# Optimization experiments

Hardware: AMD Instinct MI355X
Metric: run time of the kernel (lower is better)

The kernel has to match this reference:

```python
import jax, jax.numpy as jnp
import numpy as np

D_MODEL = 1024
N_HEADS = 16
HEAD_DIM = D_MODEL // N_HEADS


def setup_inputs() -> dict:
    key = jax.random.key(0)
    ks = jax.random.split(key, 6)
    B, S = 4, 2048
    query = jax.random.normal(ks[0], (B, S, D_MODEL), dtype=jnp.float32)
    key_value = jax.random.normal(ks[1], (B, S, D_MODEL), dtype=jnp.float32)
    scale = 1.0 / np.sqrt(D_MODEL)
    Wq = jax.random.normal(ks[2], (D_MODEL, D_MODEL), dtype=jnp.float32) * scale
    Wk = jax.random.normal(ks[3], (D_MODEL, D_MODEL), dtype=jnp.float32) * scale
    Wv = jax.random.normal(ks[4], (D_MODEL, D_MODEL), dtype=jnp.float32) * scale
    Wo = jax.random.normal(ks[5], (D_MODEL, D_MODEL), dtype=jnp.float32) * scale
    return {"query": query, "key_value": key_value, "Wq": Wq, "Wk": Wk, "Wv": Wv, "Wo": Wo}


def reference(query, key_value, Wq, Wk, Wv, Wo):
    B, S, _ = query.shape
    H, Dh = N_HEADS, HEAD_DIM
    # nn.Linear (no bias): y = x @ W.T ; then split heads -> [B, H, S, Dh]
    q = (query @ Wq.T).reshape(B, S, H, Dh).transpose(0, 2, 1, 3)
    k = (key_value @ Wk.T).reshape(B, S, H, Dh).transpose(0, 2, 1, 3)
    v = (key_value @ Wv.T).reshape(B, S, H, Dh).transpose(0, 2, 1, 3)
    scale = Dh ** -0.5
    scores = jnp.einsum("bhqd,bhkd->bhqk", q, k) * scale  # [B,H,S,S]
    causal = jnp.tril(jnp.ones((S, S), dtype=bool))  # True where allowed
    scores = jnp.where(causal, scores, -jnp.inf)
    attn = jax.nn.softmax(scores, axis=-1)
    out = jnp.einsum("bhqk,bhkd->bhqd", attn, v)  # [B,H,S,Dh]
    out = out.transpose(0, 2, 1, 3).reshape(B, S, H * Dh)
    return out @ Wo.T
```

## Files before the change

### kernel.cpp

```cpp
#include <hip/hip_runtime.h>
#include <stdint.h>

typedef unsigned short u16;
typedef __attribute__((ext_vector_type(4))) unsigned short u16x4;
typedef __attribute__((ext_vector_type(8))) unsigned short u16x8;
typedef __attribute__((ext_vector_type(8))) __bf16 bf16x8;
typedef __attribute__((ext_vector_type(2))) _Float16 half2;
typedef __attribute__((ext_vector_type(8))) _Float16 half8;
typedef __attribute__((ext_vector_type(4))) float f32x4;

#define SEQ 2048
#define DM 1024
#define NH 16
#define DH 64
#define BATCH 4
#define MROWS (BATCH * SEQ)
#define NKT 16

#define SC_LOG2E 0.18033688011112042f

__device__ __forceinline__ u16 f2bf(float f) {
    uint32_t u = __builtin_bit_cast(uint32_t, f);
    u += 0x7fffu + ((u >> 16) & 1u);
    return (u16)(u >> 16);
}
__device__ __forceinline__ u16 f2h(float f) {
    return __builtin_bit_cast(u16, (_Float16)f);
}
__device__ __forceinline__ half2 pkrtz(float a, float b) {
    return __builtin_bit_cast(half2, __builtin_amdgcn_cvt_pkrtz(a, b));
}

__device__ __forceinline__ void load16_lds(const void* g, void* l) {
    __builtin_amdgcn_global_load_lds(
        (const __attribute__((address_space(1))) uint32_t*)(uintptr_t)g,
        (__attribute__((address_space(3))) uint32_t*)(uintptr_t)l,
        16, 0, 0);
}

#define N4A (MROWS * DM / 4)
#define N4W (DM * DM / 4)

__device__ __forceinline__ void cvt_one(const float* src, u16* dst, int i) {
    float4 v = ((const float4*)src)[i];
    u16x4 o;
    o[0] = f2bf(v.x); o[1] = f2bf(v.y); o[2] = f2bf(v.z); o[3] = f2bf(v.w);
    *(u16x4*)(dst + (size_t)i * 4) = o;
}

__global__ void cvt_all(const float* __restrict__ q, const float* __restrict__ kv,
                        const float* __restrict__ w0, const float* __restrict__ w1,
                        const float* __restrict__ w2, const float* __restrict__ w3,
                        u16* __restrict__ dq, u16* __restrict__ dkv,
                        u16* __restrict__ dw0, u16* __restrict__ dw1,
                        u16* __restrict__ dw2, u16* __restrict__ dw3) {
    int i = blockIdx.x * 256 + threadIdx.x;
    if (i < N4A) { cvt_one(q, dq, i); return; }
    i -= N4A;
    if (i < N4A) { cvt_one(kv, dkv, i); return; }
    i -= N4A;
    int s = i >> 18;
    int l = i & (N4W - 1);
    const float* src = s == 0 ? w0 : s == 1 ? w1 : s == 2 ? w2 : w3;
    u16* dst = s == 0 ? dw0 : s == 1 ? dw1 : s == 2 ? dw2 : dw3;
    cvt_one(src, dst, l);
}

#define LDS_DB 24576
#define LDS_AH 8192
#define LDS_BH 4096

__device__ __forceinline__ void gemm_core(const u16* __restrict__ Ag,
                                          const u16* __restrict__ Bg,
                                          int m0, int n0, f32x4 (&acc)[4][4]) {
    __shared__ __align__(16) u16 lds[2 * LDS_DB];
    const int t = threadIdx.x;
    const int lane = t & 63;
    const int w = t >> 6;
    const int ln = lane & 15, quad = lane >> 4;
    const int wml = (w >> 1) * 64;
    const int wnl = (w & 1) * 64;
    const int rowT = t >> 2;
    const int cswz8 = (((t & 3) ^ ((t >> 3) & 3)) << 3);
    const int swz = ((quad ^ ((ln >> 1) & 3)) << 3);

    auto stageA = [&](int kt, int h, int d) {
        const u16* s = Ag + (size_t)(m0 + rowT) * DM + kt * 64 + h * 32 + cswz8;
        u16* l = &lds[d * LDS_DB + h * LDS_AH + t * 8];
        load16_lds(s, l);
        load16_lds(s + (size_t)128 * DM, l + 4096);
    };
    auto stageB = [&](int kt, int h, int d) {
        load16_lds(Bg + (size_t)(n0 + rowT) * DM + kt * 64 + h * 32 + cswz8,
                   &lds[d * LDS_DB + 2 * LDS_AH + h * LDS_BH + t * 8]);
    };

    stageA(0, 0, 0); stageB(0, 0, 0);
    stageA(0, 1, 0); stageB(0, 1, 0);
    stageA(1, 0, 1); stageB(1, 0, 1);
    asm volatile("s_waitcnt vmcnt(6)" ::: "memory");
    __builtin_amdgcn_s_barrier();

    for (int kt = 0; kt < NKT; ++kt) {
        const int d = kt & 1;
#pragma unroll
        for (int h = 0; h < 2; ++h) {
            const u16* As = &lds[d * LDS_DB + h * LDS_AH];
            const u16* Bs = &lds[d * LDS_DB + 2 * LDS_AH + h * LDS_BH];
            bf16x8 af[4], bfr[4];
#pragma unroll
            for (int mi = 0; mi < 4; ++mi)
                af[mi] = __builtin_bit_cast(bf16x8,
                    *(const u16x8*)&As[(wml + mi * 16 + ln) * 32 + swz]);
#pragma unroll
            for (int ni = 0; ni < 4; ++ni)
                bfr[ni] = __builtin_bit_cast(bf16x8,
                    *(const u16x8*)&Bs[(wnl + ni * 16 + ln) * 32 + swz]);

            if (h == 0) {
                int k1 = kt + 1 < NKT ? kt + 1 : NKT - 1;
                stageA(k1, 1, d ^ 1); stageB(k1, 1, d ^ 1);
            } else {
                int k2 = kt + 2 < NKT ? kt + 2 : NKT - 1;
                stageA(k2, 0, d); stageB(k2, 0, d);
            }

            __builtin_amdgcn_s_barrier();
            asm volatile("s_waitcnt lgkmcnt(0)" ::: "memory");
            __builtin_amdgcn_sched_barrier(0);
            __builtin_amdgcn_s_setprio(1);
#pragma unroll
            for (int mi = 0; mi < 4; ++mi)
#pragma unroll
                for (int ni = 0; ni < 4; ++ni)
                    acc[mi][ni] = __builtin_amdgcn_mfma_f32_16x16x32_bf16(
                        af[mi], bfr[ni], acc[mi][ni], 0, 0, 0);
            __builtin_amdgcn_s_setprio(0);
            __builtin_amdgcn_sched_barrier(0);
            asm volatile("s_waitcnt vmcnt(6)" ::: "memory");
            __builtin_amdgcn_s_barrier();
        }
    }
    asm volatile("s_waitcnt vmcnt(0)" ::: "memory");
}

__global__ __launch_bounds__(512, 2) void qkv_gemm(const u16* __restrict__ q_bf,
                                                   const u16* __restrict__ kv_bf,
                                                   const u16* __restrict__ wq,
                                                   const u16* __restrict__ wk,
                                                   const u16* __restrict__ wv,
                                                   u16* __restrict__ Qh,
                                                   u16* __restrict__ Kh,
                                                   u16* __restrict__ Vt) {
    const int sel = blockIdx.x >> 3;
    const int n0 = (blockIdx.x & 7) * 128;
    const int m0 = blockIdx.y * 256;
    const u16* A = (sel == 0) ? q_bf : kv_bf;
    const u16* B = (sel == 0) ? wq : (sel == 1 ? wk : wv);

    f32x4 acc[4][4] = {};
    gemm_core(A, B, m0, n0, acc);

    const int t = threadIdx.x;
    const int lane = t & 63, w = t >> 6;
    const int ln = lane & 15, quad = lane >> 4;
    const int wml = (w >> 1) * 64, wnl = (w & 1) * 64;

    if (sel == 2) {
#pragma unroll
        for (int mi = 0; mi < 4; ++mi) {
            int rowb = m0 + wml + mi * 16 + quad * 4;
            int bb = rowb >> 11, s = rowb & 2047;
#pragma unroll
            for (int ni = 0; ni < 4; ++ni) {
                int col = n0 + wnl + ni * 16 + ln;
                int h = col >> 6, d = col & 63;
                u16x4 o;
#pragma unroll
                for (int r = 0; r < 4; ++r) o[r] = f2h(acc[mi][ni][r]);
                *(u16x4*)(Vt + ((size_t)(bb * NH + h) * DH + d) * SEQ + s) = o;
            }
        }
    } else {
        u16* C = sel ? Kh : Qh;
        const float scale = sel ? 1.0f : SC_LOG2E;
#pragma unroll
        for (int mi = 0; mi < 4; ++mi) {
            int rowb = m0 + wml + mi * 16 + quad * 4;
#pragma unroll
            for (int ni = 0; ni < 4; ++ni) {
                int col = n0 + wnl + ni * 16 + ln;
                int h = col >> 6, d = col & 63;
#pragma unroll
                for (int r = 0; r < 4; ++r) {
                    int row = rowb + r;
                    int bb = row >> 11, s = row & 2047;
                    C[((size_t)((bb * NH + h) * SEQ + s) << 6) + d] = f2bf(acc[mi][ni][r] * scale);
                }
            }
        }
    }
}

__global__ __launch_bounds__(512, 2) void wo_gemm(const u16* __restrict__ A,
                                                  const u16* __restrict__ B,
                                                  float* __restrict__ Cout) {
    const int m0 = blockIdx.y * 256, n0 = blockIdx.x * 128;

    f32x4 acc[4][4] = {};
    gemm_core(A, B, m0, n0, acc);

    const int t = threadIdx.x;
    const int lane = t & 63, w = t >> 6;
    const int ln = lane & 15, quad = lane >> 4;
    const int wml = (w >> 1) * 64, wnl = (w & 1) * 64;

#pragma unroll
    for (int mi = 0; mi < 4; ++mi) {
        int rowb = m0 + wml + mi * 16 + quad * 4;
#pragma unroll
        for (int ni = 0; ni < 4; ++ni) {
            int col = n0 + wnl + ni * 16 + ln;
#pragma unroll
            for (int r = 0; r < 4; ++r)
                Cout[(size_t)(rowb + r) * DM + col] = acc[mi][ni][r];
        }
    }
}

__global__ __launch_bounds__(256) void attn_kernel(const u16* __restrict__ Q,
                                                   const u16* __restrict__ K,
                                                   const u16* __restrict__ Vt,
                                                   u16* __restrict__ AO) {
    __shared__ __align__(16) u16 qs[128 * 64];
    __shared__ __align__(16) u16 ks[64 * 64];
    __shared__ __align__(16) u16 vs[80 * 64];

    const int t = threadIdx.x;
    const int lane = t & 63, w = t >> 6;
    const int ln = lane & 15, quad = lane >> 4;
    const int l3 = ln & 7;
    const int bi = blockIdx.x;
    const int bh = bi & 63;
    const int qraw = bi >> 6;
    const int qtile = (bh & 1) ? (15 - qraw) : qraw;
    const int q0 = qtile * 128;
    const int qw0 = q0 + w * 32;
    const int ktmax = 2 * qtile + 1;
    const u16* Qb = Q + (size_t)bh * SEQ * DH;
    const u16* Kb = K + (size_t)bh * SEQ * DH;
    const u16* Vb = Vt + (size_t)bh * DH * SEQ;
    const int b = bh >> 4, h = bh & 15;

    const int cb = t & 7;
    const int r0 = t >> 3;
    const int swc = ((cb ^ (r0 & 7)) << 3);
    const int sg = ((r0 & 12) << 1) | ((r0 & 16) >> 2) | (r0 & 3);

    if (t < 128) {
        int j = t >> 3;
        u16 hv = (j == 0) ? 0x3C00 : 0;
        u16x8 o = {hv, hv, hv, hv, hv, hv, hv, hv};
        *(u16x8*)&vs[((64 + j) << 6) | (((t & 7) ^ (j & 7)) << 3)] = o;
    }

    u16x8 qreg[4];
#pragma unroll
    for (int i = 0; i < 4; ++i)
        qreg[i] = *(const u16x8*)(Qb + (size_t)(q0 + r0 + i * 32) * DH + cb * 8);
    u16x8 kreg[2], vreg[2];
#pragma unroll
    for (int i = 0; i < 2; ++i) {
        kreg[i] = *(const u16x8*)(Kb + (size_t)(i * 32 + sg) * DH + cb * 8);
        vreg[i] = *(const u16x8*)(Vb + (size_t)(r0 + i * 32) * SEQ + cb * 8);
    }

    f32x4 oaccT[2][5] = {};

    for (int kt = 0; kt <= ktmax; ++kt) {
        const int kv0 = kt * 64;
        __syncthreads();
        if (kt == 0) {
#pragma unroll
            for (int i = 0; i < 4; ++i)
                *(u16x8*)&qs[((r0 + i * 32) << 6) | swc] = qreg[i];
        }
#pragma unroll
        for (int i = 0; i < 2; ++i) {
            *(u16x8*)&ks[((r0 + i * 32) << 6) | swc] = kreg[i];
            *(u16x8*)&vs[((r0 + i * 32) << 6) | swc] = vreg[i];
        }
        __syncthreads();
        if (kt < ktmax) {
            const int kvn = kv0 + 64;
#pragma unroll
            for (int i = 0; i < 2; ++i) {
                kreg[i] = *(const u16x8*)(Kb + (size_t)(kvn + i * 32 + sg) * DH + cb * 8);
                vreg[i] = *(const u16x8*)(Vb + (size_t)(r0 + i * 32) * SEQ + kvn + cb * 8);
            }
        }

        if (kv0 >= qw0 + 32) continue;

        f32x4 st[2][4] = {};
#pragma unroll
        for (int half = 0; half < 2; ++half) {
            const int swz = (((half * 4 + quad) ^ l3) << 3);
            bf16x8 qf0 = __builtin_bit_cast(bf16x8, *(const u16x8*)&qs[((w * 32 + ln) << 6) | swz]);
            bf16x8 qf1 = __builtin_bit_cast(bf16x8, *(const u16x8*)&qs[((w * 32 + 16 + ln) << 6) | swz]);
#pragma unroll
            for (int ms = 0; ms < 4; ++ms) {
                bf16x8 kf = __builtin_bit_cast(bf16x8, *(const u16x8*)&ks[((ms * 16 + ln) << 6) | swz]);
                st[0][ms] = __builtin_amdgcn_mfma_f32_16x16x32_bf16(kf, qf0, st[0][ms], 0, 0, 0);
                st[1][ms] = __builtin_amdgcn_mfma_f32_16x16x32_bf16(kf, qf1, st[1][ms], 0, 0, 0);
            }
        }

        half8 pf[2][2];
#pragma unroll
        for (int qt2 = 0; qt2 < 2; ++qt2) {
            const int qbase = qw0 + qt2 * 16;
            if (kv0 + 63 > qbase) {
                const int relq = qbase + ln - kv0 - quad * 8;
#pragma unroll
                for (int ms = 0; ms < 4; ++ms)
#pragma unroll
                    for (int r = 0; r < 4; ++r)
                        if ((ms >> 1) * 32 + (ms & 1) * 4 + r > relq)
                            st[qt2][ms][r] = -3e38f;
            }
#pragma unroll
            for (int c = 0; c < 2; ++c) {
                half2 p0 = pkrtz(__builtin_amdgcn_exp2f(st[qt2][2 * c][0]),
                                 __builtin_amdgcn_exp2f(st[qt2][2 * c][1]));
                half2 p1 = pkrtz(__builtin_amdgcn_exp2f(st[qt2][2 * c][2]),
                                 __builtin_amdgcn_exp2f(st[qt2][2 * c][3]));
                half2 p2 = pkrtz(__builtin_amdgcn_exp2f(st[qt2][2 * c + 1][0]),
                                 __builtin_amdgcn_exp2f(st[qt2][2 * c + 1][1]));
                half2 p3 = pkrtz(__builtin_amdgcn_exp2f(st[qt2][2 * c + 1][2]),
                                 __builtin_amdgcn_exp2f(st[qt2][2 * c + 1][3]));
                half8 v;
                v[0] = p0[0]; v[1] = p0[1]; v[2] = p1[0]; v[3] = p1[1];
                v[4] = p2[0]; v[5] = p2[1]; v[6] = p3[0]; v[7] = p3[1];
                pf[qt2][c] = v;
            }
        }

#pragma unroll
        for (int c = 0; c < 2; ++c) {
            const int off = (((c * 4 + quad) ^ l3) << 3);
#pragma unroll
            for (int nd = 0; nd < 5; ++nd) {
                half8 vf = __builtin_bit_cast(half8, *(const u16x8*)&vs[((nd * 16 + ln) << 6) | off]);
                oaccT[0][nd] = __builtin_amdgcn_mfma_f32_16x16x32_f16(vf, pf[0][c], oaccT[0][nd], 0, 0, 0);
                oaccT[1][nd] = __builtin_amdgcn_mfma_f32_16x16x32_f16(vf, pf[1][c], oaccT[1][nd], 0, 0, 0);
            }
        }
    }

#pragma unroll
    for (int qt2 = 0; qt2 < 2; ++qt2) {
        float lv = __shfl(oaccT[qt2][4][0], ln, 64);
        float linv = 1.0f / lv;
        int q = q0 + w * 32 + qt2 * 16 + ln;
        size_t base = ((size_t)(b * SEQ + q) * DM) + h * DH + quad * 4;
#pragma unroll
        for (int nd = 0; nd < 4; ++nd) {
            u16x4 o;
#pragma unroll
            for (int r = 0; r < 4; ++r) o[r] = f2bf(oaccT[qt2][nd][r] * linv);
            *(u16x4*)&AO[base + nd * 16] = o;
        }
    }
}

extern "C" void kernel_launch(void* const* d_in, const int* in_sizes, int n_in,
                              void* d_out, int out_size, void* d_ws, size_t ws_size,
                              hipStream_t stream) {
    const float* query = (const float*)d_in[0];
    const float* key_value = (const float*)d_in[1];
    const float* Wq = (const float*)d_in[2];
    const float* Wk = (const float*)d_in[3];
    const float* Wv = (const float*)d_in[4];
    const float* Wo = (const float*)d_in[5];
    float* out = (float*)d_out;

    char* ws = (char*)d_ws;
    const size_t SZ_ACT = (size_t)MROWS * DM * 2;
    const size_t SZ_W = (size_t)DM * DM * 2;
    u16* q_bf  = (u16*)(ws + 0);
    u16* kv_bf = (u16*)(ws + SZ_ACT);
    u16* wq_bf = (u16*)(ws + 2 * SZ_ACT);
    u16* wk_bf = (u16*)(ws + 2 * SZ_ACT + SZ_W);
    u16* wv_bf = (u16*)(ws + 2 * SZ_ACT + 2 * SZ_W);
    u16* wo_bf = (u16*)(ws + 2 * SZ_ACT + 3 * SZ_W);
    u16* Qh    = (u16*)(ws + 2 * SZ_ACT + 4 * SZ_W);
    u16* Kh    = (u16*)(ws + 2 * SZ_ACT + 4 * SZ_W + SZ_ACT);
    u16* Vt    = (u16*)(ws + 2 * SZ_ACT + 4 * SZ_W + 2 * SZ_ACT);
    u16* AOb   = q_bf;

    const int n4_total = 2 * N4A + 4 * N4W;
    cvt_all<<<n4_total / 256, 256, 0, stream>>>(query, key_value, Wq, Wk, Wv, Wo,
                                                q_bf, kv_bf, wq_bf, wk_bf, wv_bf, wo_bf);

    qkv_gemm<<<dim3(24, MROWS / 256), 512, 0, stream>>>(q_bf, kv_bf, wq_bf, wk_bf, wv_bf,
                                                        Qh, Kh, Vt);

    attn_kernel<<<1024, 256, 0, stream>>>(Qh, Kh, Vt, AOb);

    wo_gemm<<<dim3(DM / 128, MROWS / 256), 512, 0, stream>>>(AOb, wo_bf, out);
}
```

Baseline: 272.4 us.

## Switch projection GEMMs to 256x256 tiles with XCD-aware block mapping

Replaces the 256x128 GEMM core with a 256x256 tile core. It uses 8 waves with 128x64 per-wave subtiles, a quarter-tile interleaved schedule of LDS reads, global-to-LDS stages and MFMA bursts, and an XOR swizzle over 64-wide rows. The QKV and Wo launches become 1D grids with an XCD-aware mapping so each XCD works on a contiguous group of M tiles. The goal is more arithmetic per loaded byte and better L2 locality. The cost is twice the accumulator registers and 128KB of LDS, which limits occupancy, plus fewer blocks (128 for Wo) on a 256-CU device.

```diff
diff --git a/kernel.cpp b/kernel.cpp
--- a/kernel.cpp
+++ b/kernel.cpp
@@ -66,80 +66,153 @@
     cvt_one(src, dst, l);
 }
 
-#define LDS_DB 24576
-#define LDS_AH 8192
-#define LDS_BH 4096
-
-__device__ __forceinline__ void gemm_core(const u16* __restrict__ Ag,
-                                          const u16* __restrict__ Bg,
-                                          int m0, int n0, f32x4 (&acc)[4][4]) {
-    __shared__ __align__(16) u16 lds[2 * LDS_DB];
+__device__ __forceinline__ void gemm256_core(const u16* __restrict__ Ag,
+                                             const u16* __restrict__ Bg,
+                                             int m0, int n0,
+                                             f32x4 (&acc)[8][4]) {
+    __shared__ __align__(16) u16 lds[4 * 16384];
     const int t = threadIdx.x;
     const int lane = t & 63;
     const int w = t >> 6;
     const int ln = lane & 15, quad = lane >> 4;
-    const int wml = (w >> 1) * 64;
-    const int wnl = (w & 1) * 64;
-    const int rowT = t >> 2;
-    const int cswz8 = (((t & 3) ^ ((t >> 3) & 3)) << 3);
-    const int swz = ((quad ^ ((ln >> 1) & 3)) << 3);
-
-    auto stageA = [&](int kt, int h, int d) {
-        const u16* s = Ag + (size_t)(m0 + rowT) * DM + kt * 64 + h * 32 + cswz8;
-        u16* l = &lds[d * LDS_DB + h * LDS_AH + t * 8];
-        load16_lds(s, l);
-        load16_lds(s + (size_t)128 * DM, l + 4096);
+    const int wm2 = w >> 2;
+    const int wn4 = w & 3;
+    const int schunk = (((t & 7) ^ ((t >> 3) & 7)) << 3);
+
+    auto stage = [&](int tb, int h, int d, int kt) {
+        const u16* base = tb ? Bg : Ag;
+        const int g0 = (tb ? n0 : m0) + h * 128 + (t >> 3);
+        const u16* src = base + (size_t)g0 * DM + kt * 64 + schunk;
+        u16* dst = &lds[(d * 2 + tb) * 16384 + h * 8192 + t * 8];
+        load16_lds(src, dst);
+        load16_lds(src + (size_t)64 * DM, dst + 4096);
     };
-    auto stageB = [&](int kt, int h, int d) {
-        load16_lds(Bg + (size_t)(n0 + rowT) * DM + kt * 64 + h * 32 + cswz8,
-                   &lds[d * LDS_DB + 2 * LDS_AH + h * LDS_BH + t * 8]);
+    auto rdA = [&](int d, int qr, int ks, int mi) -> bf16x8 {
+        const int row = wm2 * 128 + qr * 64 + mi * 16 + ln;
+        return __builtin_bit_cast(bf16x8, *(const u16x8*)&lds[
+            (d * 2) * 16384 + row * 64 + (((ks * 4 + quad) ^ (row & 7)) << 3)]);
     };
-
-    stageA(0, 0, 0); stageB(0, 0, 0);
-    stageA(0, 1, 0); stageB(0, 1, 0);
-    stageA(1, 0, 1); stageB(1, 0, 1);
-    asm volatile("s_waitcnt vmcnt(6)" ::: "memory");
+    auto rdB = [&](int d, int qc, int ks, int nj) -> bf16x8 {
+        const int row = wn4 * 64 + qc * 32 + nj * 16 + ln;
+        return __builtin_bit_cast(bf16x8, *(const u16x8*)&lds[
+            (d * 2 + 1) * 16384 + row * 64 + (((ks * 4 + quad) ^ (row & 7)) << 3)]);
+    };
+
+    bf16x8 ar[2][4], br[2][2][2];
+
+    auto qmfma = [&](int qr, int qc) {
+#pragma unroll
+        for (int ks = 0; ks < 2; ++ks)
+#pragma unroll
+            for (int mi = 0; mi < 4; ++mi)
+#pragma unroll
+                for (int nj = 0; nj < 2; ++nj)
+                    acc[qr * 4 + mi][qc * 2 + nj] =
+                        __builtin_amdgcn_mfma_f32_16x16x32_bf16(
+                            ar[ks][mi], br[qc][ks][nj],
+                            acc[qr * 4 + mi][qc * 2 + nj], 0, 0, 0);
+    };
+
+    stage(0, 0, 0, 0); stage(0, 1, 0, 0);
+    stage(1, 0, 0, 0); stage(1, 1, 0, 0);
+    stage(1, 0, 1, 1); stage(1, 1, 1, 1);
+    asm volatile("s_waitcnt vmcnt(4)" ::: "memory");
     __builtin_amdgcn_s_barrier();
 
-    for (int kt = 0; kt < NKT; ++kt) {
-        const int d = kt & 1;
-#pragma unroll
-        for (int h = 0; h < 2; ++h) {
-            const u16* As = &lds[d * LDS_DB + h * LDS_AH];
-            const u16* Bs = &lds[d * LDS_DB + 2 * LDS_AH + h * LDS_BH];
-            bf16x8 af[4], bfr[4];
-#pragma unroll
-            for (int mi = 0; mi < 4; ++mi)
-                af[mi] = __builtin_bit_cast(bf16x8,
-                    *(const u16x8*)&As[(wml + mi * 16 + ln) * 32 + swz]);
-#pragma unroll
-            for (int ni = 0; ni < 4; ++ni)
-                bfr[ni] = __builtin_bit_cast(bf16x8,
-                    *(const u16x8*)&Bs[(wnl + ni * 16 + ln) * 32 + swz]);
-
-            if (h == 0) {
-                int k1 = kt + 1 < NKT ? kt + 1 : NKT - 1;
-                stageA(k1, 1, d ^ 1); stageB(k1, 1, d ^ 1);
-            } else {
-                int k2 = kt + 2 < NKT ? kt + 2 : NKT - 1;
-                stageA(k2, 0, d); stageB(k2, 0, d);
-            }
-
-            __builtin_amdgcn_s_barrier();
-            asm volatile("s_waitcnt lgkmcnt(0)" ::: "memory");
-            __builtin_amdgcn_sched_barrier(0);
-            __builtin_amdgcn_s_setprio(1);
-#pragma unroll
-            for (int mi = 0; mi < 4; ++mi)
-#pragma unroll
-                for (int ni = 0; ni < 4; ++ni)
-                    acc[mi][ni] = __builtin_amdgcn_mfma_f32_16x16x32_bf16(
-                        af[mi], bfr[ni], acc[mi][ni], 0, 0, 0);
-            __builtin_amdgcn_s_setprio(0);
-            __builtin_amdgcn_sched_barrier(0);
-            asm volatile("s_waitcnt vmcnt(6)" ::: "memory");
-            __builtin_amdgcn_s_barrier();
-        }
+    for (int j = 0; j < NKT / 2; ++j) {
+        const int ktB = 2 * j + 1;
+        const int ktC = 2 * j + 2;
+        const int ktD = 2 * j + 3;
+        const bool pre = (j < NKT / 2 - 1);
+
+#pragma unroll
+        for (int ks = 0; ks < 2; ++ks) {
+#pragma unroll
+            for (int mi = 0; mi < 4; ++mi) ar[ks][mi] = rdA(0, 0, ks, mi);
+#pragma unroll
+            for (int nj = 0; nj < 2; ++nj) br[0][ks][nj] = rdB(0, 0, ks, nj);
+        }
+        stage(0, 0, 1, ktB);
+        __builtin_amdgcn_s_barrier();
+        __builtin_amdgcn_s_setprio(1);
+        qmfma(0, 0);
+        __builtin_amdgcn_s_setprio(0);
+        __builtin_amdgcn_s_barrier();
+
+#pragma unroll
+        for (int ks = 0; ks < 2; ++ks)
+#pragma unroll
+            for (int nj = 0; nj < 2; ++nj) br[1][ks][nj] = rdB(0, 1, ks, nj);
+        stage(0, 1, 1, ktB);
+        __builtin_amdgcn_s_barrier();
+        __builtin_amdgcn_s_setprio(1);
+        qmfma(0, 1);
+        __builtin_amdgcn_s_setprio(0);
+        __builtin_amdgcn_s_barrier();
+
+#pragma unroll
+        for (int ks = 0; ks < 2; ++ks)
+#pragma unroll
+            for (int mi = 0; mi < 4; ++mi) ar[ks][mi] = rdA(0, 1, ks, mi);
+        if (pre) stage(1, 0, 0, ktC);
+        __builtin_amdgcn_s_barrier();
+        __builtin_amdgcn_s_setprio(1);
+        qmfma(1, 1);
+        __builtin_amdgcn_s_setprio(0);
+        __builtin_amdgcn_s_barrier();
+
+        if (pre) stage(1, 1, 0, ktC);
+        __builtin_amdgcn_s_barrier();
+        __builtin_amdgcn_s_setprio(1);
+        qmfma(1, 0);
+        __builtin_amdgcn_s_setprio(0);
+        if (pre) { asm volatile("s_waitcnt vmcnt(4)" ::: "memory"); }
+        else     { asm volatile("s_waitcnt vmcnt(0)" ::: "memory"); }
+        __builtin_amdgcn_s_barrier();
+
+#pragma unroll
+        for (int ks = 0; ks < 2; ++ks) {
+#pragma unroll
+            for (int mi = 0; mi < 4; ++mi) ar[ks][mi] = rdA(1, 0, ks, mi);
+#pragma unroll
+            for (int nj = 0; nj < 2; ++nj) br[0][ks][nj] = rdB(1, 0, ks, nj);
+        }
+        if (pre) stage(0, 0, 0, ktC);
+        __builtin_amdgcn_s_barrier();
+        __builtin_amdgcn_s_setprio(1);
+        qmfma(0, 0);
+        __builtin_amdgcn_s_setprio(0);
+        __builtin_amdgcn_s_barrier();
+
+#pragma unroll
+        for (int ks = 0; ks < 2; ++ks)
+#pragma unroll
+            for (int nj = 0; nj < 2; ++nj) br[1][ks][nj] = rdB(1, 1, ks, nj);
+        if (pre) stage(0, 1, 0, ktC);
+        __builtin_amdgcn_s_barrier();
+        __builtin_amdgcn_s_setprio(1);
+        qmfma(0, 1);
+        __builtin_amdgcn_s_setprio(0);
+        __builtin_amdgcn_s_barrier();
+
+#pragma unroll
+        for (int ks = 0; ks < 2; ++ks)
+#pragma unroll
+            for (int mi = 0; mi < 4; ++mi) ar[ks][mi] = rdA(1, 1, ks, mi);
+        if (pre) stage(1, 0, 1, ktD);
+        __builtin_amdgcn_s_barrier();
+        __builtin_amdgcn_s_setprio(1);
+        qmfma(1, 1);
+        __builtin_amdgcn_s_setprio(0);
+        __builtin_amdgcn_s_barrier();
+
+        if (pre) stage(1, 1, 1, ktD);
+        __builtin_amdgcn_s_barrier();
+        __builtin_amdgcn_s_setprio(1);
+        qmfma(1, 0);
+        __builtin_amdgcn_s_setprio(0);
+        asm volatile("s_waitcnt vmcnt(4)" ::: "memory");
+        __builtin_amdgcn_s_barrier();
     }
     asm volatile("s_waitcnt vmcnt(0)" ::: "memory");
 }
@@ -152,28 +225,31 @@
                                                    u16* __restrict__ Qh,
                                                    u16* __restrict__ Kh,
                                                    u16* __restrict__ Vt) {
-    const int sel = blockIdx.x >> 3;
-    const int n0 = (blockIdx.x & 7) * 128;
-    const int m0 = blockIdx.y * 256;
+    const int g = blockIdx.x;
+    const int xcd = g & 7, l = g >> 3;
+    const int mt = xcd * 4 + (l & 3);
+    const int np = l >> 2;
+    const int sel = np >> 2;
+    const int m0 = mt * 256, n0 = (np & 3) * 256;
     const u16* A = (sel == 0) ? q_bf : kv_bf;
     const u16* B = (sel == 0) ? wq : (sel == 1 ? wk : wv);
 
-    f32x4 acc[4][4] = {};
-    gemm_core(A, B, m0, n0, acc);
+    f32x4 acc[8][4] = {};
+    gemm256_core(A, B, m0, n0, acc);
 
     const int t = threadIdx.x;
     const int lane = t & 63, w = t >> 6;
     const int ln = lane & 15, quad = lane >> 4;
-    const int wml = (w >> 1) * 64, wnl = (w & 1) * 64;
+    const int wm2 = w >> 2, wn4 = w & 3;
 
     if (sel == 2) {
 #pragma unroll
-        for (int mi = 0; mi < 4; ++mi) {
-            int rowb = m0 + wml + mi * 16 + quad * 4;
+        for (int mi = 0; mi < 8; ++mi) {
+            int rowb = m0 + wm2 * 128 + mi * 16 + quad * 4;
             int bb = rowb >> 11, s = rowb & 2047;
 #pragma unroll
             for (int ni = 0; ni < 4; ++ni) {
-                int col = n0 + wnl + ni * 16 + ln;
+                int col = n0 + wn4 * 64 + ni * 16 + ln;
                 int h = col >> 6, d = col & 63;
                 u16x4 o;
 #pragma unroll
@@ -185,11 +261,11 @@
         u16* C = sel ? Kh : Qh;
         const float scale = sel ? 1.0f : SC_LOG2E;
 #pragma unroll
-        for (int mi = 0; mi < 4; ++mi) {
-            int rowb = m0 + wml + mi * 16 + quad * 4;
+        for (int mi = 0; mi < 8; ++mi) {
+            int rowb = m0 + wm2 * 128 + mi * 16 + quad * 4;
 #pragma unroll
             for (int ni = 0; ni < 4; ++ni) {
-                int col = n0 + wnl + ni * 16 + ln;
+                int col = n0 + wn4 * 64 + ni * 16 + ln;
                 int h = col >> 6, d = col & 63;
 #pragma unroll
                 for (int r = 0; r < 4; ++r) {
@@ -205,22 +281,26 @@
 __global__ __launch_bounds__(512, 2) void wo_gemm(const u16* __restrict__ A,
                                                   const u16* __restrict__ B,
                                                   float* __restrict__ Cout) {
-    const int m0 = blockIdx.y * 256, n0 = blockIdx.x * 128;
-
-    f32x4 acc[4][4] = {};
-    gemm_core(A, B, m0, n0, acc);
+    const int g = blockIdx.x;
+    const int xcd = g & 7, l = g >> 3;
+    const int mt = xcd * 4 + (l & 3);
+    const int nt = l >> 2;
+    const int m0 = mt * 256, n0 = nt * 256;
+
+    f32x4 acc[8][4] = {};
+    gemm256_core(A, B, m0, n0, acc);
 
     const int t = threadIdx.x;
     const int lane = t & 63, w = t >> 6;
     const int ln = lane & 15, quad = lane >> 4;
-    const int wml = (w >> 1) * 64, wnl = (w & 1) * 64;
-
-#pragma unroll
-    for (int mi = 0; mi < 4; ++mi) {
-        int rowb = m0 + wml + mi * 16 + quad * 4;
+    const int wm2 = w >> 2, wn4 = w & 3;
+
+#pragma unroll
+    for (int mi = 0; mi < 8; ++mi) {
+        int rowb = m0 + wm2 * 128 + mi * 16 + quad * 4;
 #pragma unroll
         for (int ni = 0; ni < 4; ++ni) {
-            int col = n0 + wnl + ni * 16 + ln;
+            int col = n0 + wn4 * 64 + ni * 16 + ln;
 #pragma unroll
             for (int r = 0; r < 4; ++r)
                 Cout[(size_t)(rowb + r) * DM + col] = acc[mi][ni][r];
@@ -403,10 +483,10 @@
     cvt_all<<<n4_total / 256, 256, 0, stream>>>(query, key_value, Wq, Wk, Wv, Wo,
                                                 q_bf, kv_bf, wq_bf, wk_bf, wv_bf, wo_bf);
 
-    qkv_gemm<<<dim3(24, MROWS / 256), 512, 0, stream>>>(q_bf, kv_bf, wq_bf, wk_bf, wv_bf,
-                                                        Qh, Kh, Vt);
+    qkv_gemm<<<384, 512, 0, stream>>>(q_bf, kv_bf, wq_bf, wk_bf, wv_bf,
+                                      Qh, Kh, Vt);
 
     attn_kernel<<<1024, 256, 0, stream>>>(Qh, Kh, Vt, AOb);
 
-    wo_gemm<<<dim3(DM / 128, MROWS / 256), 512, 0, stream>>>(AOb, wo_bf, out);
-}
+    wo_gemm<<<128, 512, 0, stream>>>(AOb, wo_bf, out);
+}
```

Result: no change. 269.6 us (-1.0%).

## Rewrite GEMM core as templated 4-wave kernel with quadrant MFMA interleave and XCD remap

Applied to the files above, without the earlier changes.

Replaces the 8-wave, 64-deep-k GEMM core with a templated 4-wave core that uses a 32-deep k step. Each wave computes a larger output tile, split into quadrants whose MFMAs are interleaved with LDS reads and global-to-LDS prefetches. Block indices are remapped so that neighbouring M tiles land on the same XCD, which should improve L2 reuse. The Wo GEMM moves to 128x128 tiles with 3 blocks per CU. Gains come from higher register-level reuse and better overlap, at the cost of more register pressure and more barriers per k step.

```diff
diff --git a/kernel.cpp b/kernel.cpp
--- a/kernel.cpp
+++ b/kernel.cpp
@@ -15,7 +15,6 @@
 #define DH 64
 #define BATCH 4
 #define MROWS (BATCH * SEQ)
-#define NKT 16
 
 #define SC_LOG2E 0.18033688011112042f
 
@@ -66,85 +65,100 @@
     cvt_one(src, dst, l);
 }
 
-#define LDS_DB 24576
-#define LDS_AH 8192
-#define LDS_BH 4096
-
-__device__ __forceinline__ void gemm_core(const u16* __restrict__ Ag,
-                                          const u16* __restrict__ Bg,
-                                          int m0, int n0, f32x4 (&acc)[4][4]) {
-    __shared__ __align__(16) u16 lds[2 * LDS_DB];
+template<int BM, int BN>
+__device__ __forceinline__ void gemm_core2(const u16* __restrict__ Ag,
+                                           const u16* __restrict__ Bg,
+                                           int m0, int n0,
+                                           f32x4 (&acc)[BM / 32][BN / 32]) {
+    constexpr int MI = BM / 32, NJ = BN / 32;
+    constexpr int LA = BM / 64;
+    constexpr int L = LA + BN / 64;
+    constexpr int BUF = (BM + BN) * 32;
+    constexpr int KT = DM / 32;
+    __shared__ __align__(16) u16 lds[2 * BUF];
     const int t = threadIdx.x;
-    const int lane = t & 63;
-    const int w = t >> 6;
+    const int lane = t & 63, w = t >> 6;
     const int ln = lane & 15, quad = lane >> 4;
-    const int wml = (w >> 1) * 64;
-    const int wnl = (w & 1) * 64;
-    const int rowT = t >> 2;
-    const int cswz8 = (((t & 3) ^ ((t >> 3) & 3)) << 3);
-    const int swz = ((quad ^ ((ln >> 1) & 3)) << 3);
-
-    auto stageA = [&](int kt, int h, int d) {
-        const u16* s = Ag + (size_t)(m0 + rowT) * DM + kt * 64 + h * 32 + cswz8;
-        u16* l = &lds[d * LDS_DB + h * LDS_AH + t * 8];
-        load16_lds(s, l);
-        load16_lds(s + (size_t)128 * DM, l + 4096);
+    const int wrow = (w >> 1) * (BM / 2), wcol = (w & 1) * (BN / 2);
+    const int rdchunk = ((quad ^ ((ln >> 1) & 3)) << 3);
+    const int schunk = (((t & 3) ^ ((t >> 3) & 3)) << 3);
+    const int srow = t >> 2;
+
+    auto stage1 = [&](int kt, int d, int i) {
+        if (kt >= KT) kt = KT - 1;
+        const u16* base = (i < LA) ? Ag : Bg;
+        const int seg = (i < LA) ? i : i - LA;
+        const int g0 = ((i < LA) ? m0 : n0) + seg * 64 + srow;
+        const int dst = d * BUF + ((i < LA) ? 0 : BM * 32) + seg * 2048 + t * 8;
+        load16_lds(base + (size_t)g0 * DM + kt * 32 + schunk, &lds[dst]);
     };
-    auto stageB = [&](int kt, int h, int d) {
-        load16_lds(Bg + (size_t)(n0 + rowT) * DM + kt * 64 + h * 32 + cswz8,
-                   &lds[d * LDS_DB + 2 * LDS_AH + h * LDS_BH + t * 8]);
+    auto rdA = [&](int c, int mi) -> bf16x8 {
+        const int row = wrow + mi * 16 + ln;
+        return __builtin_bit_cast(bf16x8,
+            *(const u16x8*)&lds[c * BUF + row * 32 + rdchunk]);
     };
-
-    stageA(0, 0, 0); stageB(0, 0, 0);
-    stageA(0, 1, 0); stageB(0, 1, 0);
-    stageA(1, 0, 1); stageB(1, 0, 1);
-    asm volatile("s_waitcnt vmcnt(6)" ::: "memory");
+    auto rdB = [&](int c, int nj) -> bf16x8 {
+        const int row = wcol + nj * 16 + ln;
+        return __builtin_bit_cast(bf16x8,
+            *(const u16x8*)&lds[c * BUF + BM * 32 + row * 32 + rdchunk]);
+    };
+
+    bf16x8 ar[MI / 2], br[2][NJ / 2];
+    auto qm = [&](int qr, int qc) {
+#pragma unroll
+        for (int mi = 0; mi < MI / 2; ++mi)
+#pragma unroll
+            for (int nj = 0; nj < NJ / 2; ++nj)
+                acc[qr * (MI / 2) + mi][qc * (NJ / 2) + nj] =
+                    __builtin_amdgcn_mfma_f32_16x16x32_bf16(
+                        ar[mi], br[qc][nj],
+                        acc[qr * (MI / 2) + mi][qc * (NJ / 2) + nj], 0, 0, 0);
+    };
+
+#pragma unroll
+    for (int i = 0; i < L; ++i) stage1(0, 0, i);
+    stage1(1, 1, 0); stage1(1, 1, 1);
+    asm volatile("s_waitcnt vmcnt(2)" ::: "memory");
     __builtin_amdgcn_s_barrier();
 
-    for (int kt = 0; kt < NKT; ++kt) {
-        const int d = kt & 1;
-#pragma unroll
-        for (int h = 0; h < 2; ++h) {
-            const u16* As = &lds[d * LDS_DB + h * LDS_AH];
-            const u16* Bs = &lds[d * LDS_DB + 2 * LDS_AH + h * LDS_BH];
-            bf16x8 af[4], bfr[4];
-#pragma unroll
-            for (int mi = 0; mi < 4; ++mi)
-                af[mi] = __builtin_bit_cast(bf16x8,
-                    *(const u16x8*)&As[(wml + mi * 16 + ln) * 32 + swz]);
-#pragma unroll
-            for (int ni = 0; ni < 4; ++ni)
-                bfr[ni] = __builtin_bit_cast(bf16x8,
-                    *(const u16x8*)&Bs[(wnl + ni * 16 + ln) * 32 + swz]);
-
-            if (h == 0) {
-                int k1 = kt + 1 < NKT ? kt + 1 : NKT - 1;
-                stageA(k1, 1, d ^ 1); stageB(k1, 1, d ^ 1);
-            } else {
-                int k2 = kt + 2 < NKT ? kt + 2 : NKT - 1;
-                stageA(k2, 0, d); stageB(k2, 0, d);
-            }
-
-            __builtin_amdgcn_s_barrier();
-            asm volatile("s_waitcnt lgkmcnt(0)" ::: "memory");
-            __builtin_amdgcn_sched_barrier(0);
-            __builtin_amdgcn_s_setprio(1);
-#pragma unroll
-            for (int mi = 0; mi < 4; ++mi)
-#pragma unroll
-                for (int ni = 0; ni < 4; ++ni)
-                    acc[mi][ni] = __builtin_amdgcn_mfma_f32_16x16x32_bf16(
-                        af[mi], bfr[ni], acc[mi][ni], 0, 0, 0);
-            __builtin_amdgcn_s_setprio(0);
-            __builtin_amdgcn_sched_barrier(0);
-            asm volatile("s_waitcnt vmcnt(6)" ::: "memory");
-            __builtin_amdgcn_s_barrier();
-        }
+    for (int kt = 0; kt < KT; ++kt) {
+        const int c = kt & 1, o = c ^ 1;
+#pragma unroll
+        for (int mi = 0; mi < MI / 2; ++mi) ar[mi] = rdA(c, mi);
+#pragma unroll
+        for (int nj = 0; nj < NJ / 2; ++nj) br[0][nj] = rdB(c, nj);
+        if constexpr (L == 6) { stage1(kt + 1, o, 2); stage1(kt + 1, o, 3); }
+        else                  { stage1(kt + 1, o, 2); }
+        __builtin_amdgcn_s_barrier();
+        asm volatile("s_waitcnt lgkmcnt(0)" ::: "memory");
+        __builtin_amdgcn_sched_barrier(0);
+        __builtin_amdgcn_s_setprio(1); qm(0, 0); __builtin_amdgcn_s_setprio(0);
+        __builtin_amdgcn_s_barrier();
+#pragma unroll
+        for (int nj = 0; nj < NJ / 2; ++nj) br[1][nj] = rdB(c, NJ / 2 + nj);
+        if constexpr (L == 6) { stage1(kt + 1, o, 4); stage1(kt + 1, o, 5); }
+        else                  { stage1(kt + 1, o, 3); }
+        __builtin_amdgcn_s_barrier();
+        asm volatile("s_waitcnt lgkmcnt(0)" ::: "memory");
+        __builtin_amdgcn_sched_barrier(0);
+        __builtin_amdgcn_s_setprio(1); qm(0, 1); __builtin_amdgcn_s_setprio(0);
+        __builtin_amdgcn_s_barrier();
+#pragma unroll
+        for (int mi = 0; mi < MI / 2; ++mi) ar[mi] = rdA(c, MI / 2 + mi);
+        __builtin_amdgcn_s_barrier();
+        asm volatile("s_waitcnt lgkmcnt(0)" ::: "memory");
+        __builtin_amdgcn_sched_barrier(0);
+        __builtin_amdgcn_s_setprio(1); qm(1, 1); __builtin_amdgcn_s_setprio(0);
+        __builtin_amdgcn_s_barrier();
+        stage1(kt + 2, c, 0); stage1(kt + 2, c, 1);
+        __builtin_amdgcn_s_setprio(1); qm(1, 0); __builtin_amdgcn_s_setprio(0);
+        asm volatile("s_waitcnt vmcnt(2)" ::: "memory");
+        __builtin_amdgcn_s_barrier();
     }
     asm volatile("s_waitcnt vmcnt(0)" ::: "memory");
 }
 
-__global__ __launch_bounds__(512, 2) void qkv_gemm(const u16* __restrict__ q_bf,
+__global__ __launch_bounds__(256, 2) void qkv_gemm(const u16* __restrict__ q_bf,
                                                    const u16* __restrict__ kv_bf,
                                                    const u16* __restrict__ wq,
                                                    const u16* __restrict__ wk,
@@ -152,28 +166,31 @@
                                                    u16* __restrict__ Qh,
                                                    u16* __restrict__ Kh,
                                                    u16* __restrict__ Vt) {
-    const int sel = blockIdx.x >> 3;
-    const int n0 = (blockIdx.x & 7) * 128;
-    const int m0 = blockIdx.y * 256;
+    const int g = blockIdx.x;
+    const int xcd = g & 7, l = g >> 3;
+    const int mt = xcd * 4 + (l & 3);
+    const int np = l >> 2;
+    const int sel = np >> 3;
+    const int m0 = mt * 256, n0 = (np & 7) * 128;
     const u16* A = (sel == 0) ? q_bf : kv_bf;
     const u16* B = (sel == 0) ? wq : (sel == 1 ? wk : wv);
 
-    f32x4 acc[4][4] = {};
-    gemm_core(A, B, m0, n0, acc);
+    f32x4 acc[8][4] = {};
+    gemm_core2<256, 128>(A, B, m0, n0, acc);
 
     const int t = threadIdx.x;
     const int lane = t & 63, w = t >> 6;
     const int ln = lane & 15, quad = lane >> 4;
-    const int wml = (w >> 1) * 64, wnl = (w & 1) * 64;
+    const int wrow = (w >> 1) * 128, wcol = (w & 1) * 64;
 
     if (sel == 2) {
 #pragma unroll
-        for (int mi = 0; mi < 4; ++mi) {
-            int rowb = m0 + wml + mi * 16 + quad * 4;
+        for (int mi = 0; mi < 8; ++mi) {
+            int rowb = m0 + wrow + mi * 16 + quad * 4;
             int bb = rowb >> 11, s = rowb & 2047;
 #pragma unroll
             for (int ni = 0; ni < 4; ++ni) {
-                int col = n0 + wnl + ni * 16 + ln;
+                int col = n0 + wcol + ni * 16 + ln;
                 int h = col >> 6, d = col & 63;
                 u16x4 o;
 #pragma unroll
@@ -185,11 +202,11 @@
         u16* C = sel ? Kh : Qh;
         const float scale = sel ? 1.0f : SC_LOG2E;
 #pragma unroll
-        for (int mi = 0; mi < 4; ++mi) {
-            int rowb = m0 + wml + mi * 16 + quad * 4;
+        for (int mi = 0; mi < 8; ++mi) {
+            int rowb = m0 + wrow + mi * 16 + quad * 4;
 #pragma unroll
             for (int ni = 0; ni < 4; ++ni) {
-                int col = n0 + wnl + ni * 16 + ln;
+                int col = n0 + wcol + ni * 16 + ln;
                 int h = col >> 6, d = col & 63;
 #pragma unroll
                 for (int r = 0; r < 4; ++r) {
@@ -202,25 +219,29 @@
     }
 }
 
-__global__ __launch_bounds__(512, 2) void wo_gemm(const u16* __restrict__ A,
+__global__ __launch_bounds__(256, 3) void wo_gemm(const u16* __restrict__ A,
                                                   const u16* __restrict__ B,
                                                   float* __restrict__ Cout) {
-    const int m0 = blockIdx.y * 256, n0 = blockIdx.x * 128;
+    const int g = blockIdx.x;
+    const int xcd = g & 7, l = g >> 3;
+    const int mt = xcd * 8 + (l & 7);
+    const int nt = l >> 3;
+    const int m0 = mt * 128, n0 = nt * 128;
 
     f32x4 acc[4][4] = {};
-    gemm_core(A, B, m0, n0, acc);
+    gemm_core2<128, 128>(A, B, m0, n0, acc);
 
     const int t = threadIdx.x;
     const int lane = t & 63, w = t >> 6;
     const int ln = lane & 15, quad = lane >> 4;
-    const int wml = (w >> 1) * 64, wnl = (w & 1) * 64;
+    const int wrow = (w >> 1) * 64, wcol = (w & 1) * 64;
 
 #pragma unroll
     for (int mi = 0; mi < 4; ++mi) {
-        int rowb = m0 + wml + mi * 16 + quad * 4;
+        int rowb = m0 + wrow + mi * 16 + quad * 4;
 #pragma unroll
         for (int ni = 0; ni < 4; ++ni) {
-            int col = n0 + wnl + ni * 16 + ln;
+            int col = n0 + wcol + ni * 16 + ln;
 #pragma unroll
             for (int r = 0; r < 4; ++r)
                 Cout[(size_t)(rowb + r) * DM + col] = acc[mi][ni][r];
@@ -403,10 +424,10 @@
     cvt_all<<<n4_total / 256, 256, 0, stream>>>(query, key_value, Wq, Wk, Wv, Wo,
                                                 q_bf, kv_bf, wq_bf, wk_bf, wv_bf, wo_bf);
 
-    qkv_gemm<<<dim3(24, MROWS / 256), 512, 0, stream>>>(q_bf, kv_bf, wq_bf, wk_bf, wv_bf,
-                                                        Qh, Kh, Vt);
+    qkv_gemm<<<768, 256, 0, stream>>>(q_bf, kv_bf, wq_bf, wk_bf, wv_bf,
+                                      Qh, Kh, Vt);
 
     attn_kernel<<<1024, 256, 0, stream>>>(Qh, Kh, Vt, AOb);
 
-    wo_gemm<<<dim3(DM / 128, MROWS / 256), 512, 0, stream>>>(AOb, wo_bf, out);
-}
+    wo_gemm<<<512, 256, 0, stream>>>(AOb, wo_bf, out);
+}
```

Measured after the change: 263.7 us. -3.2%, faster.
